# Performance work log

Measured on AMD Instinct MI355X. Metric: run time of the kernel, lower is better.

Reference implementation:

```python
import jax, jax.numpy as jnp
import numpy as np

B, C, T, F = 16, 2, 2000, 257

def setup_inputs() -> dict:
    key = jax.random.key(0)
    k1, = jax.random.split(key, 1)
    inp = jax.random.normal(k1, (B, C, T, F, 2), dtype=jnp.float32)
    s_1 = jnp.zeros((B, 1, F, 1), dtype=jnp.float32)
    weights = jnp.ones((1, C, 1, F, 1), dtype=jnp.float32)
    bias = jnp.zeros((1, C, 1, F, 1), dtype=jnp.float32)
    alpha_param = jnp.full((1, 1, F, 1), -4.0, dtype=jnp.float32)
    return {"input": inp, "s_1": s_1, "weights": weights, "bias": bias, "alpha_param": alpha_param}

def reference(input, s_1, weights, bias, alpha_param):
    # input: [B, C, T, F, 2]
    in_data2 = jnp.sum(input ** 2, axis=-1, keepdims=True)       # [B, C, T, F, 1]
    alpha = jax.nn.sigmoid(alpha_param)                           # [1, 1, F, 1]
    x_seq = jnp.moveaxis(in_data2[:, 0:1], 2, 0)                  # [T, B, 1, F, 1]

    def step(s, xt):
        s_new = s * (1.0 - alpha) + xt * alpha                    # [B, 1, F, 1]
        return s_new, s_new

    s_final, smooth = jax.lax.scan(step, s_1, x_seq)              # smooth: [T, B, 1, F, 1]
    smooth_data = jnp.sqrt(jnp.moveaxis(smooth, 0, 2))            # [B, 1, T, F, 1]
    cat_data = jnp.concatenate([smooth_data, jnp.sqrt(in_data2[:, 1:])], axis=1)  # [B, C, T, F, 1]
    res = input / (cat_data + 1e-8) * weights + bias              # [B, C, T, F, 2]
    return res, s_final, smooth_data
```

## Files before the change

kernel.cpp:

```cpp
#include <hip/hip_runtime.h>
#include <math.h>

#define B 16
#define C 2
#define T 2000
#define F 257
#define NC 50
#define L  (T / NC)

#define RES_SIZE   (B * C * T * F * 2)
#define OFF_SFINAL (RES_SIZE)
#define OFF_SMOOTH (RES_SIZE + B * F)

__device__ __forceinline__ float sigmoidf_(float x) {
    return 1.0f / (1.0f + expf(-x));
}

__global__ void k_carries(const float* __restrict__ input,
                          const float* __restrict__ alpha_param,
                          float* __restrict__ carry) {
    int tid = blockIdx.x * blockDim.x + threadIdx.x;
    const int N = B * F * NC;
    if (tid >= N) return;
    int f = tid % F;
    int r = tid / F;
    int c = r % NC;
    int b = r / NC;

    float a = sigmoidf_(alpha_param[f]);
    float beta = 1.0f - a;

    const float2* inp = (const float2*)input + ((size_t)(b * C + 0) * T + (size_t)c * L) * F + f;
    float s = 0.0f;
#pragma unroll 8
    for (int t = 0; t < L; ++t) {
        float2 v = inp[(size_t)t * F];
        float x = v.x * v.x + v.y * v.y;
        s = beta * s + a * x;
    }
    carry[(b * NC + c) * F + f] = s;
}

__global__ void k_scan(const float* __restrict__ s_1,
                       const float* __restrict__ alpha_param,
                       const float* __restrict__ carry,
                       float* __restrict__ chunkstart,
                       float* __restrict__ out) {
    int tid = blockIdx.x * blockDim.x + threadIdx.x;
    const int N = B * F;
    if (tid >= N) return;
    int f = tid % F;
    int b = tid / F;

    float a = sigmoidf_(alpha_param[f]);
    float beta = 1.0f - a;
    float bL = 1.0f;
#pragma unroll
    for (int i = 0; i < L; ++i) bL *= beta;

    float s = s_1[b * F + f];
    for (int c = 0; c < NC; ++c) {
        int idx = (b * NC + c) * F + f;
        chunkstart[idx] = s;
        s = bL * s + carry[idx];
    }
    out[OFF_SFINAL + b * F + f] = s;
}

__global__ void k_final0(const float* __restrict__ input,
                         const float* __restrict__ alpha_param,
                         const float* __restrict__ weights,
                         const float* __restrict__ bias,
                         const float* __restrict__ chunkstart,
                         float* __restrict__ out) {
    int tid = blockIdx.x * blockDim.x + threadIdx.x;
    const int N = B * F * NC;
    if (tid >= N) return;
    int f = tid % F;
    int r = tid / F;
    int c = r % NC;
    int b = r / NC;

    float a = sigmoidf_(alpha_param[f]);
    float beta = 1.0f - a;
    float w0 = weights[0 * F + f];
    float b0 = bias[0 * F + f];

    const float2* inp = (const float2*)input + ((size_t)(b * C + 0) * T + (size_t)c * L) * F + f;
    float2* res = (float2*)out + ((size_t)(b * C + 0) * T + (size_t)c * L) * F + f;
    float* smooth = out + OFF_SMOOTH + ((size_t)b * T + (size_t)c * L) * F + f;

    float s = chunkstart[(b * NC + c) * F + f];
#pragma unroll 8
    for (int t = 0; t < L; ++t) {
        float2 v = inp[(size_t)t * F];
        float x = v.x * v.x + v.y * v.y;
        s = beta * s + a * x;
        float sm = sqrtf(s);
        float inv = 1.0f / (sm + 1e-8f);
        float2 rr;
        rr.x = v.x * inv * w0 + b0;
        rr.y = v.y * inv * w0 + b0;
        res[(size_t)t * F] = rr;
        smooth[(size_t)t * F] = sm;
    }
}

__global__ void k_final1(const float* __restrict__ input,
                         const float* __restrict__ weights,
                         const float* __restrict__ bias,
                         float* __restrict__ out) {
    int tid = blockIdx.x * blockDim.x + threadIdx.x;
    const int N = B * T * F;
    if (tid >= N) return;
    int f = tid % F;
    int r = tid / F;
    int t = r % T;
    int b = r / T;

    float w1 = weights[1 * F + f];
    float b1 = bias[1 * F + f];

    const float2* inp = (const float2*)input + ((size_t)(b * C + 1) * T + t) * F + f;
    float2* res = (float2*)out + ((size_t)(b * C + 1) * T + t) * F + f;

    float2 v = *inp;
    float x = v.x * v.x + v.y * v.y;
    float sm = sqrtf(x);
    float inv = 1.0f / (sm + 1e-8f);
    float2 rr;
    rr.x = v.x * inv * w1 + b1;
    rr.y = v.y * inv * w1 + b1;
    *res = rr;
}

extern "C" void kernel_launch(void* const* d_in, const int* in_sizes, int n_in,
                              void* d_out, int out_size, void* d_ws, size_t ws_size,
                              hipStream_t stream) {
    const float* input       = (const float*)d_in[0];
    const float* s_1         = (const float*)d_in[1];
    const float* weights     = (const float*)d_in[2];
    const float* bias        = (const float*)d_in[3];
    const float* alpha_param = (const float*)d_in[4];
    float* out = (float*)d_out;

    float* carry      = (float*)d_ws;
    float* chunkstart = (float*)d_ws + B * NC * F;

    const int N1 = B * F * NC;
    const int N2 = B * F;
    const int N3 = B * T * F;

    k_carries<<<(N1 + 255) / 256, 256, 0, stream>>>(input, alpha_param, carry);
    k_scan<<<(N2 + 255) / 256, 256, 0, stream>>>(s_1, alpha_param, carry, chunkstart, out);
    k_final0<<<(N1 + 255) / 256, 256, 0, stream>>>(input, alpha_param, weights, bias, chunkstart, out);
    k_final1<<<(N3 + 255) / 256, 256, 0, stream>>>(input, weights, bias, out);
}
```

Baseline: 300.4 us.

## Merge scan into final pass and co-schedule channel-1 normalization with carries

Reduces four launches to two. The channel-1 normalization now runs as extra blocks inside the carry kernel and uses float4 vectorized loads and stores. The separate serial scan kernel is removed: each chunk thread of the final pass rebuilds its own start state from the prefix of carries, with a 4-way unrolled recurrence. The chunk count rises from 50 to 100 for more parallelism, at the cost of quadratic redundant carry reads and possible small floating-point differences from reassociation.

```diff
diff --git a/kernel.cpp b/kernel.cpp
--- a/kernel.cpp
+++ b/kernel.cpp
@@ -5,23 +5,89 @@
 #define C 2
 #define T 2000
 #define F 257
-#define NC 50
+#define NC 100
 #define L  (T / NC)
 
 #define RES_SIZE   (B * C * T * F * 2)
 #define OFF_SFINAL (RES_SIZE)
 #define OFF_SMOOTH (RES_SIZE + B * F)
 
+#define N_CARRY (B * NC * F)
+#define G0      ((N_CARRY + 255) / 256)
+#define SLAB4   (T * F * 2 / 4)
+#define N_V4    (B * SLAB4)
+#define G1      ((N_V4 + 255) / 256)
+
 __device__ __forceinline__ float sigmoidf_(float x) {
     return 1.0f / (1.0f + expf(-x));
 }
 
-__global__ void k_carries(const float* __restrict__ input,
-                          const float* __restrict__ alpha_param,
-                          float* __restrict__ carry) {
-    int tid = blockIdx.x * blockDim.x + threadIdx.x;
-    const int N = B * F * NC;
-    if (tid >= N) return;
+__global__ __launch_bounds__(256) void k_phase1(const float* __restrict__ input,
+                                                const float* __restrict__ alpha_param,
+                                                const float* __restrict__ weights,
+                                                const float* __restrict__ bias,
+                                                float* __restrict__ carry,
+                                                float* __restrict__ out) {
+    int bid = blockIdx.x;
+    if (bid < G0) {
+        int tid = bid * 256 + threadIdx.x;
+        if (tid >= N_CARRY) return;
+        int f = tid % F;
+        int r = tid / F;
+        int c = r % NC;
+        int b = r / NC;
+
+        float a = sigmoidf_(alpha_param[f]);
+        float beta = 1.0f - a;
+
+        const float2* inp = (const float2*)input
+                          + ((size_t)(b * C + 0) * T + (size_t)c * L) * F + f;
+        float s = 0.0f;
+#pragma unroll
+        for (int t = 0; t < L; ++t) {
+            float2 v = inp[(size_t)t * F];
+            s = beta * s + a * (v.x * v.x + v.y * v.y);
+        }
+        carry[((size_t)b * NC + c) * F + f] = s;
+    } else {
+        int idx = (bid - G0) * 256 + threadIdx.x;
+        if (idx >= N_V4) return;
+        int b   = idx / SLAB4;
+        int rem = idx - b * SLAB4;
+
+        const float4* ip = (const float4*)(input + ((size_t)(b * C + 1) * T) * F * 2) + rem;
+        float4 v = *ip;
+
+        int e  = rem * 2;
+        int f0 = e % F;
+        int f1 = (f0 + 1 == F) ? 0 : (f0 + 1);
+
+        float w0 = weights[F + f0], w1 = weights[F + f1];
+        float q0 = bias[F + f0],    q1 = bias[F + f1];
+
+        float inv0 = 1.0f / (sqrtf(v.x * v.x + v.y * v.y) + 1e-8f);
+        float inv1 = 1.0f / (sqrtf(v.z * v.z + v.w * v.w) + 1e-8f);
+
+        float4 rr;
+        rr.x = v.x * inv0 * w0 + q0;
+        rr.y = v.y * inv0 * w0 + q0;
+        rr.z = v.z * inv1 * w1 + q1;
+        rr.w = v.w * inv1 * w1 + q1;
+
+        float4* rp = (float4*)(out + ((size_t)(b * C + 1) * T) * F * 2) + rem;
+        *rp = rr;
+    }
+}
+
+__global__ __launch_bounds__(256) void k_phase2(const float* __restrict__ input,
+                                                const float* __restrict__ s_1,
+                                                const float* __restrict__ alpha_param,
+                                                const float* __restrict__ weights,
+                                                const float* __restrict__ bias,
+                                                const float* __restrict__ carry,
+                                                float* __restrict__ out) {
+    int tid = blockIdx.x * 256 + threadIdx.x;
+    if (tid >= N_CARRY) return;
     int f = tid % F;
     int r = tid / F;
     int c = r % NC;
@@ -29,69 +95,35 @@
 
     float a = sigmoidf_(alpha_param[f]);
     float beta = 1.0f - a;
-
-    const float2* inp = (const float2*)input + ((size_t)(b * C + 0) * T + (size_t)c * L) * F + f;
-    float s = 0.0f;
-#pragma unroll 8
-    for (int t = 0; t < L; ++t) {
-        float2 v = inp[(size_t)t * F];
-        float x = v.x * v.x + v.y * v.y;
-        s = beta * s + a * x;
-    }
-    carry[(b * NC + c) * F + f] = s;
-}
-
-__global__ void k_scan(const float* __restrict__ s_1,
-                       const float* __restrict__ alpha_param,
-                       const float* __restrict__ carry,
-                       float* __restrict__ chunkstart,
-                       float* __restrict__ out) {
-    int tid = blockIdx.x * blockDim.x + threadIdx.x;
-    const int N = B * F;
-    if (tid >= N) return;
-    int f = tid % F;
-    int b = tid / F;
-
-    float a = sigmoidf_(alpha_param[f]);
-    float beta = 1.0f - a;
     float bL = 1.0f;
 #pragma unroll
     for (int i = 0; i < L; ++i) bL *= beta;
+    float bL2 = bL * bL;
+    float bL3 = bL2 * bL;
+    float bL4 = bL2 * bL2;
 
+    const float* cp = carry + (size_t)b * NC * F + f;
     float s = s_1[b * F + f];
-    for (int c = 0; c < NC; ++c) {
-        int idx = (b * NC + c) * F + f;
-        chunkstart[idx] = s;
-        s = bL * s + carry[idx];
+    int j = 0;
+    for (; j + 4 <= c; j += 4) {
+        float c0 = cp[(size_t)(j    ) * F];
+        float c1 = cp[(size_t)(j + 1) * F];
+        float c2 = cp[(size_t)(j + 2) * F];
+        float c3 = cp[(size_t)(j + 3) * F];
+        s = fmaf(bL4, s, fmaf(bL3, c0, fmaf(bL2, c1, fmaf(bL, c2, c3))));
     }
-    out[OFF_SFINAL + b * F + f] = s;
-}
+    for (; j < c; ++j) s = fmaf(bL, s, cp[(size_t)j * F]);
 
-__global__ void k_final0(const float* __restrict__ input,
-                         const float* __restrict__ alpha_param,
-                         const float* __restrict__ weights,
-                         const float* __restrict__ bias,
-                         const float* __restrict__ chunkstart,
-                         float* __restrict__ out) {
-    int tid = blockIdx.x * blockDim.x + threadIdx.x;
-    const int N = B * F * NC;
-    if (tid >= N) return;
-    int f = tid % F;
-    int r = tid / F;
-    int c = r % NC;
-    int b = r / NC;
+    float w0 = weights[f];
+    float q0 = bias[f];
 
-    float a = sigmoidf_(alpha_param[f]);
-    float beta = 1.0f - a;
-    float w0 = weights[0 * F + f];
-    float b0 = bias[0 * F + f];
-
-    const float2* inp = (const float2*)input + ((size_t)(b * C + 0) * T + (size_t)c * L) * F + f;
-    float2* res = (float2*)out + ((size_t)(b * C + 0) * T + (size_t)c * L) * F + f;
+    const float2* inp = (const float2*)input
+                      + ((size_t)(b * C + 0) * T + (size_t)c * L) * F + f;
+    float2* res = (float2*)out
+                + ((size_t)(b * C + 0) * T + (size_t)c * L) * F + f;
     float* smooth = out + OFF_SMOOTH + ((size_t)b * T + (size_t)c * L) * F + f;
 
-    float s = chunkstart[(b * NC + c) * F + f];
-#pragma unroll 8
+#pragma unroll
     for (int t = 0; t < L; ++t) {
         float2 v = inp[(size_t)t * F];
         float x = v.x * v.x + v.y * v.y;
@@ -99,39 +131,12 @@
         float sm = sqrtf(s);
         float inv = 1.0f / (sm + 1e-8f);
         float2 rr;
-        rr.x = v.x * inv * w0 + b0;
-        rr.y = v.y * inv * w0 + b0;
+        rr.x = v.x * inv * w0 + q0;
+        rr.y = v.y * inv * w0 + q0;
         res[(size_t)t * F] = rr;
         smooth[(size_t)t * F] = sm;
     }
-}
-
-__global__ void k_final1(const float* __restrict__ input,
-                         const float* __restrict__ weights,
-                         const float* __restrict__ bias,
-                         float* __restrict__ out) {
-    int tid = blockIdx.x * blockDim.x + threadIdx.x;
-    const int N = B * T * F;
-    if (tid >= N) return;
-    int f = tid % F;
-    int r = tid / F;
-    int t = r % T;
-    int b = r / T;
-
-    float w1 = weights[1 * F + f];
-    float b1 = bias[1 * F + f];
-
-    const float2* inp = (const float2*)input + ((size_t)(b * C + 1) * T + t) * F + f;
-    float2* res = (float2*)out + ((size_t)(b * C + 1) * T + t) * F + f;
-
-    float2 v = *inp;
-    float x = v.x * v.x + v.y * v.y;
-    float sm = sqrtf(x);
-    float inv = 1.0f / (sm + 1e-8f);
-    float2 rr;
-    rr.x = v.x * inv * w1 + b1;
-    rr.y = v.y * inv * w1 + b1;
-    *res = rr;
+    if (c == NC - 1) out[OFF_SFINAL + (size_t)b * F + f] = s;
 }
 
 extern "C" void kernel_launch(void* const* d_in, const int* in_sizes, int n_in,
@@ -144,15 +149,8 @@
     const float* alpha_param = (const float*)d_in[4];
     float* out = (float*)d_out;
 
-    float* carry      = (float*)d_ws;
-    float* chunkstart = (float*)d_ws + B * NC * F;
+    float* carry = (float*)d_ws;
 
-    const int N1 = B * F * NC;
-    const int N2 = B * F;
-    const int N3 = B * T * F;
-
-    k_carries<<<(N1 + 255) / 256, 256, 0, stream>>>(input, alpha_param, carry);
-    k_scan<<<(N2 + 255) / 256, 256, 0, stream>>>(s_1, alpha_param, carry, chunkstart, out);
-    k_final0<<<(N1 + 255) / 256, 256, 0, stream>>>(input, alpha_param, weights, bias, chunkstart, out);
-    k_final1<<<(N3 + 255) / 256, 256, 0, stream>>>(input, weights, bias, out);
+    k_phase1<<<G0 + G1, 256, 0, stream>>>(input, alpha_param, weights, bias, carry, out);
+    k_phase2<<<G0, 256, 0, stream>>>(input, s_1, alpha_param, weights, bias, carry, out);
 }
```

Result: no change. 299.8 us (-0.2%).
